# Performance work log

Hardware: AMD Instinct MI355X
Metric: run time of the kernel (lower is better)

## Reference

```python
import jax, jax.numpy as jnp
import numpy as np

H = 1024      # hidden_size
NH = 16       # num_heads
HD = H // NH  # head_dim
E = 4096      # expand_size
EPS = 1e-5


def layernorm(x, w, b):
    mu = jnp.mean(x, axis=-1, keepdims=True)
    var = jnp.mean(jnp.square(x - mu), axis=-1, keepdims=True)
    return (x - mu) * jax.lax.rsqrt(var + EPS) * w + b


def setup_inputs() -> dict:
    key = jax.random.key(0)
    ks = jax.random.split(key, 8)
    s = 1.0 / np.sqrt(H)
    return {
        "x": jax.random.normal(ks[0], (4, 2048, H), dtype=jnp.float32),
        "ln1_w": jnp.ones((H,), jnp.float32),
        "ln1_b": jnp.zeros((H,), jnp.float32),
        "Wqkv": jax.random.normal(ks[1], (H, 3 * H), dtype=jnp.float32) * s,
        "bqkv": jnp.zeros((3 * H,), jnp.float32),
        "Wo": jax.random.normal(ks[2], (H, H), dtype=jnp.float32) * s,
        "bo": jnp.zeros((H,), jnp.float32),
        "ln2_w": jnp.ones((H,), jnp.float32),
        "ln2_b": jnp.zeros((H,), jnp.float32),
        "fc1_w": jax.random.normal(ks[3], (H, E), dtype=jnp.float32) * s,
        "fc1_b": jnp.zeros((E,), jnp.float32),
        "fc2_w": jax.random.normal(ks[4], (E, H), dtype=jnp.float32) * (1.0 / np.sqrt(E)),
        "fc2_b": jnp.zeros((H,), jnp.float32),
    }


def reference(x, ln1_w, ln1_b, Wqkv, bqkv, Wo, bo, ln2_w, ln2_b, fc1_w, fc1_b, fc2_w, fc2_b):
    B, S, C = x.shape
    # --- attention sub-block (pre-norm) ---
    h = layernorm(x, ln1_w, ln1_b)
    qkv = h @ Wqkv + bqkv                             # [B,S,3C]
    qkv = qkv.reshape(B, S, 3, NH, HD)
    q, k, v = (jnp.moveaxis(qkv[:, :, i], 2, 1) for i in range(3))  # [B,NH,S,HD]
    attn = jnp.einsum("bhqd,bhkd->bhqk", q, k) / np.sqrt(HD)        # [B,NH,S,S]
    attn = jax.nn.softmax(attn, axis=-1)
    o = jnp.einsum("bhqk,bhkd->bhqd", attn, v)        # [B,NH,S,HD]
    o = jnp.moveaxis(o, 1, 2).reshape(B, S, C)
    x = x + o @ Wo + bo
    # --- FFN sub-block (pre-norm) ---
    h = layernorm(x, ln2_w, ln2_b)
    h = jax.nn.gelu(h @ fc1_w + fc1_b, approximate=False)
    return x + h @ fc2_w + fc2_b
```

## Files before the change

kernel.cpp:

```cpp
#include <hip/hip_runtime.h>
#include <hip/hip_bf16.h>
#include <math.h>

typedef __bf16 bf16_t;
typedef __bf16 bf16x4 __attribute__((ext_vector_type(4)));
typedef short  s16x8  __attribute__((ext_vector_type(8)));
typedef float  f32x4  __attribute__((ext_vector_type(4)));
typedef float  f32x16 __attribute__((ext_vector_type(16)));

#define DEVINL __device__ __forceinline__

DEVINL void gload_lds16(const void* g, void* l) {
  __builtin_amdgcn_global_load_lds(
      (const __attribute__((address_space(1))) unsigned int*)g,
      (__attribute__((address_space(3))) unsigned int*)l, 16, 0, 0);
}

DEVINL f32x4 mfma16(s16x8 a, s16x8 b, f32x4 c) {
  return __builtin_amdgcn_mfma_f32_16x16x32_bf16(a, b, c, 0, 0, 0);
}

DEVINL f32x16 mfma32(s16x8 a, s16x8 b, f32x16 c) {
  return __builtin_amdgcn_mfma_f32_32x32x16_bf16(a, b, c, 0, 0, 0);
}

DEVINL float fexp2(float x) { return __builtin_amdgcn_exp2f(x); }

__global__ __launch_bounds__(256) void tcast_kernel(const float* __restrict__ W,
                                                    bf16_t* __restrict__ WT,
                                                    int K, int N) {
  __shared__ float tile[32][33];
  const int n0 = blockIdx.x * 32, k0 = blockIdx.y * 32;
  const int tx = threadIdx.x, ty = threadIdx.y;
#pragma unroll
  for (int j = 0; j < 4; ++j)
    tile[ty + j * 8][tx] = W[(size_t)(k0 + ty + j * 8) * N + (n0 + tx)];
  __syncthreads();
#pragma unroll
  for (int j = 0; j < 4; ++j)
    WT[(size_t)(n0 + ty + j * 8) * K + (k0 + tx)] = (bf16_t)tile[tx][ty + j * 8];
}

__global__ __launch_bounds__(256) void ln_kernel(const float* __restrict__ x,
                                                 const float* __restrict__ w,
                                                 const float* __restrict__ b,
                                                 bf16_t* __restrict__ out) {
  const int row = blockIdx.x, tid = threadIdx.x;
  const float4 v = ((const float4*)(x + (size_t)row * 1024))[tid];
  float s  = v.x + v.y + v.z + v.w;
  float s2 = v.x * v.x + v.y * v.y + v.z * v.z + v.w * v.w;
#pragma unroll
  for (int off = 32; off > 0; off >>= 1) {
    s  += __shfl_down(s, off);
    s2 += __shfl_down(s2, off);
  }
  __shared__ float red[8];
  const int wave = tid >> 6, lane = tid & 63;
  if (lane == 0) { red[wave] = s; red[4 + wave] = s2; }
  __syncthreads();
  s  = red[0] + red[1] + red[2] + red[3];
  s2 = red[4] + red[5] + red[6] + red[7];
  const float mu = s * (1.0f / 1024.0f);
  const float rs = rsqrtf(s2 * (1.0f / 1024.0f) - mu * mu + 1e-5f);
  const float4 wv = ((const float4*)w)[tid];
  const float4 bv = ((const float4*)b)[tid];
  bf16x4 o;
  o[0] = (bf16_t)((v.x - mu) * rs * wv.x + bv.x);
  o[1] = (bf16_t)((v.y - mu) * rs * wv.y + bv.y);
  o[2] = (bf16_t)((v.z - mu) * rs * wv.z + bv.z);
  o[3] = (bf16_t)((v.w - mu) * rs * wv.w + bv.w);
  ((bf16x4*)(out + (size_t)row * 1024))[tid] = o;
}

template <int EPI>
__global__ __launch_bounds__(256, 4) void gemm128b(const bf16_t* __restrict__ A,
                                                   const bf16_t* __restrict__ BT,
                                                   const float* __restrict__ bias,
                                                   const float* __restrict__ resid,
                                                   void* __restrict__ out,
                                                   void* __restrict__ out2,
                                                   int M, int N, int K) {
  __shared__ __align__(16) bf16_t sA[128 * 64];
  __shared__ __align__(16) bf16_t sB[128 * 64];
  const int tid = threadIdx.x;
  const int lane = tid & 63, wave = tid >> 6;
  const int wr = wave >> 1, wc = wave & 1;
  const int g = lane >> 4, lr = lane & 15;

  const int bid = blockIdx.x;
  const int cpx = gridDim.x >> 3;
  const int gid = (bid & 7) * cpx + (bid >> 3);
  const int m0 = (gid & 63) * 128, n0 = (gid >> 6) * 128;
  const bf16_t* Ab = A + (size_t)m0 * K;
  const bf16_t* Bb = BT + (size_t)n0 * K;

  f32x4 acc[4][4] = {};

  for (int kt = 0; kt < K; kt += 64) {
    __syncthreads();
#pragma unroll
    for (int q = 0; q < 4; ++q) {
      const int c = q * 256 + tid;
      const int r = c >> 3;
      const int j = (c & 7) ^ (r & 7);
      const size_t doff = (size_t)(q * 256 + wave * 64) * 8;
      gload_lds16(Ab + (size_t)r * K + kt + j * 8, sA + doff);
      gload_lds16(Bb + (size_t)r * K + kt + j * 8, sB + doff);
    }
    __syncthreads();
#pragma unroll
    for (int ks = 0; ks < 2; ++ks) {
      s16x8 af[4], bfr[4];
#pragma unroll
      for (int m = 0; m < 4; ++m) {
        const int r = wr * 64 + m * 16 + lr;
        af[m] = *(const s16x8*)&sA[r * 64 + (((ks << 2) + g) ^ (r & 7)) * 8];
      }
#pragma unroll
      for (int n = 0; n < 4; ++n) {
        const int r = wc * 64 + n * 16 + lr;
        bfr[n] = *(const s16x8*)&sB[r * 64 + (((ks << 2) + g) ^ (r & 7)) * 8];
      }
#pragma unroll
      for (int m = 0; m < 4; ++m)
#pragma unroll
        for (int n = 0; n < 4; ++n)
          acc[m][n] = mfma16(af[m], bfr[n], acc[m][n]);
    }
  }

#pragma unroll
  for (int m = 0; m < 4; ++m)
#pragma unroll
    for (int n = 0; n < 4; ++n) {
      const int col = n0 + wc * 64 + n * 16 + lr;
      const float bv = bias[col];
      const int rrow0 = m0 + wr * 64 + m * 16 + g * 4;
      if (EPI == 3 && col >= 2048) {
        const int col2 = col - 2048;
        bf16x4 pk;
#pragma unroll
        for (int i = 0; i < 4; ++i) pk[i] = (bf16_t)(acc[m][n][i] + bv);
        const size_t didx =
            ((((size_t)(rrow0 >> 11)) * 16 + (col2 >> 6)) * 64 + (col2 & 63)) * 2048 +
            (rrow0 & 2047);
        *(bf16x4*)&((bf16_t*)out2)[didx] = pk;
      } else {
#pragma unroll
        for (int i = 0; i < 4; ++i) {
          const int rrow = rrow0 + i;
          float v = acc[m][n][i] + bv;
          if (EPI == 1) {
            const size_t idx = (size_t)rrow * N + col;
            v += resid[idx];
            ((float*)out)[idx] = v;
          } else if (EPI == 2) {
            v = 0.5f * v * (1.0f + erff(v * 0.70710678118f));
            ((bf16_t*)out)[(size_t)rrow * N + col] = (bf16_t)v;
          } else if (EPI == 3) {
            ((bf16_t*)out)[(size_t)rrow * 2048 + col] = (bf16_t)v;
          } else {
            ((bf16_t*)out)[(size_t)rrow * N + col] = (bf16_t)v;
          }
        }
      }
    }
}

__global__ __launch_bounds__(256) void flash_attn8(const bf16_t* __restrict__ qk,
                                                   const bf16_t* __restrict__ vt,
                                                   bf16_t* __restrict__ O) {
  const int S = 2048;
  const int bid = blockIdx.x;
  const int swz = (bid & 7) * 128 + (bid >> 3);
  const int bh = swz >> 4;
  const int qt = swz & 15;
  const int h = bh & 15;
  const size_t rowbase = (size_t)(bh >> 4) * S;
  const int tid = threadIdx.x, lane = tid & 63, wave = tid >> 6;
  const int ql = lane & 31;
  const int H = lane >> 5;
  const int q0w = qt * 128 + wave * 32;
  const float c2 = 0.18033688f;

  __shared__ __align__(16) bf16_t sK[64 * 64];
  __shared__ __align__(16) bf16_t sVT[64 * 64];
  __shared__ __align__(16) bf16_t sP[4][32 * 64];

  const bf16_t* vtb = vt + (size_t)bh * 64 * 2048;

  s16x8 qf[4];
  {
    const bf16_t* qrow = qk + (rowbase + q0w + ql) * 2048 + h * 64 + 8 * H;
#pragma unroll
    for (int ks = 0; ks < 4; ++ks) qf[ks] = *(const s16x8*)(qrow + 16 * ks);
  }

  f32x16 oa[2] = {};
  float m2 = -1e30f, lrun = 0.0f;

  for (int kv0 = 0; kv0 < S; kv0 += 64) {
    __syncthreads();
#pragma unroll
    for (int p = 0; p < 2; ++p) {
      const int c = p * 256 + wave * 64 + lane;
      const int r = c >> 3;
      const int pb = (c & 7) ^ (r & 7);
      char* dK = (char*)sK + (size_t)(p * 256 + wave * 64) * 16;
      char* dV = (char*)sVT + (size_t)(p * 256 + wave * 64) * 16;
      gload_lds16(qk + (rowbase + kv0 + r) * 2048 + 1024 + h * 64 + pb * 8, dK);
      gload_lds16(vtb + (size_t)r * 2048 + kv0 + pb * 8, dV);
    }
    __syncthreads();

    f32x16 sc[2] = {};
#pragma unroll
    for (int ks = 0; ks < 4; ++ks)
#pragma unroll
      for (int kvf = 0; kvf < 2; ++kvf) {
        const int R = kvf * 32 + ql;
        const s16x8 ak = *(const s16x8*)&sK[R * 64 + (((2 * ks + H) ^ (R & 7)) * 8)];
        sc[kvf] = mfma32(ak, qf[ks], sc[kvf]);
      }

    float rmax = sc[0][0];
#pragma unroll
    for (int f = 0; f < 2; ++f)
#pragma unroll
      for (int r = 0; r < 16; ++r) rmax = fmaxf(rmax, sc[f][r]);
    rmax = fmaxf(rmax, __shfl_xor(rmax, 32));
    const float pm2 = rmax * c2;
    if (!__all(pm2 <= m2 + 8.0f)) {
      const float mn = fmaxf(m2, pm2);
      const float alpha = fexp2(m2 - mn);
      m2 = mn;
      lrun *= alpha;
#pragma unroll
      for (int f = 0; f < 2; ++f)
#pragma unroll
        for (int r = 0; r < 16; ++r) oa[f][r] *= alpha;
    }
    float rsum = 0.0f;
#pragma unroll
    for (int f = 0; f < 2; ++f)
#pragma unroll
      for (int r = 0; r < 16; ++r) {
        const float pp = fexp2(fmaf(sc[f][r], c2, -m2));
        sc[f][r] = pp;
        rsum += pp;
      }
    rsum += __shfl_xor(rsum, 32);
    lrun += rsum;

#pragma unroll
    for (int ks = 0; ks < 4; ++ks)
#pragma unroll
      for (int hi = 0; hi < 2; ++hi) {
        const int f = ks >> 1, rb = 8 * (ks & 1) + 4 * hi;
        bf16x4 pk;
#pragma unroll
        for (int e = 0; e < 4; ++e) pk[e] = (bf16_t)sc[f][rb + e];
        const int slot = ((2 * ks + hi) + ql) & 7;
        *(bf16x4*)&sP[wave][ql * 64 + slot * 8 + 4 * H] = pk;
      }

#pragma unroll
    for (int ks = 0; ks < 4; ++ks) {
      const s16x8 pbf = *(const s16x8*)&sP[wave][ql * 64 + (((2 * ks + H) + ql) & 7) * 8];
#pragma unroll
      for (int df = 0; df < 2; ++df) {
        const int R = df * 32 + ql;
        const s16x8 va = *(const s16x8*)&sVT[R * 64 + (((2 * ks + H) ^ (R & 7)) * 8)];
        oa[df] = mfma32(va, pbf, oa[df]);
      }
    }
  }

  const float rl = 1.0f / lrun;
#pragma unroll
  for (int df = 0; df < 2; ++df)
#pragma unroll
    for (int rr = 0; rr < 4; ++rr) {
      bf16x4 ov;
#pragma unroll
      for (int e = 0; e < 4; ++e) ov[e] = (bf16_t)(oa[df][4 * rr + e] * rl);
      const int d0 = 32 * df + 8 * rr + 4 * H;
      *(bf16x4*)&O[(rowbase + q0w + ql) * 1024 + h * 64 + d0] = ov;
    }
}

extern "C" void kernel_launch(void* const* d_in, const int* in_sizes, int n_in,
                              void* d_out, int out_size, void* d_ws, size_t ws_size,
                              hipStream_t stream) {
  const float* x    = (const float*)d_in[0];
  const float* ln1w = (const float*)d_in[1];
  const float* ln1b = (const float*)d_in[2];
  const float* Wqkv = (const float*)d_in[3];
  const float* bqkv = (const float*)d_in[4];
  const float* Wo   = (const float*)d_in[5];
  const float* bo   = (const float*)d_in[6];
  const float* ln2w = (const float*)d_in[7];
  const float* ln2b = (const float*)d_in[8];
  const float* fc1w = (const float*)d_in[9];
  const float* fc1b = (const float*)d_in[10];
  const float* fc2w = (const float*)d_in[11];
  const float* fc2b = (const float*)d_in[12];

  const int M = 8192;

  char* ws = (char*)d_ws;
  size_t off = 0;
  auto alloc = [&](size_t bytes) {
    char* p = ws + off;
    off += (bytes + 255) & ~(size_t)255;
    return p;
  };
  bf16_t* WqkvT = (bf16_t*)alloc((size_t)3072 * 1024 * 2);
  bf16_t* WoT   = (bf16_t*)alloc((size_t)1024 * 1024 * 2);
  bf16_t* fc1T  = (bf16_t*)alloc((size_t)4096 * 1024 * 2);
  bf16_t* fc2T  = (bf16_t*)alloc((size_t)1024 * 4096 * 2);
  bf16_t* h1    = (bf16_t*)alloc((size_t)M * 1024 * 2);
  bf16_t* qkQK  = (bf16_t*)alloc((size_t)M * 2048 * 2);
  bf16_t* vTg   = (bf16_t*)alloc((size_t)M * 1024 * 2);
  bf16_t* attnO = (bf16_t*)alloc((size_t)M * 1024 * 2);
  float*  x2    = (float*)alloc((size_t)M * 1024 * 4);
  bf16_t* h2   = h1;
  bf16_t* gbuf = qkQK;
  if (off > ws_size) return;

  const dim3 tb(32, 8);
  tcast_kernel<<<dim3(96, 32), tb, 0, stream>>>(Wqkv, WqkvT, 1024, 3072);
  tcast_kernel<<<dim3(32, 32), tb, 0, stream>>>(Wo, WoT, 1024, 1024);
  tcast_kernel<<<dim3(128, 32), tb, 0, stream>>>(fc1w, fc1T, 1024, 4096);
  tcast_kernel<<<dim3(32, 128), tb, 0, stream>>>(fc2w, fc2T, 4096, 1024);

  ln_kernel<<<M, 256, 0, stream>>>(x, ln1w, ln1b, h1);

  gemm128b<3><<<dim3(1536), 256, 0, stream>>>(h1, WqkvT, bqkv, nullptr, qkQK, vTg, M, 3072, 1024);

  flash_attn8<<<dim3(1024), 256, 0, stream>>>(qkQK, vTg, attnO);

  gemm128b<1><<<dim3(512), 256, 0, stream>>>(attnO, WoT, bo, x, x2, nullptr, M, 1024, 1024);

  ln_kernel<<<M, 256, 0, stream>>>(x2, ln2w, ln2b, h2);

  gemm128b<2><<<dim3(2048), 256, 0, stream>>>(h2, fc1T, fc1b, nullptr, gbuf, nullptr, M, 4096, 1024);

  gemm128b<1><<<dim3(512), 256, 0, stream>>>(gbuf, fc2T, fc2b, x2, (float*)d_out, nullptr, M, 1024, 4096);
}
```

Before: 433.3 us.

## Double-buffer LDS tiles in GEMM to overlap global loads with MFMA compute

Converts the bf16 GEMM kernel to use two LDS buffers for the A and B tiles. It issues the async global-to-LDS load for the next K tile before computing on the current one, and drops to one barrier per iteration. The aim is to hide global memory latency behind MFMA work. In exchange LDS per block doubles to 64KB and launch bounds drop from 4 to 2 blocks per SM, which lowers occupancy.

```diff
diff --git a/kernel.cpp b/kernel.cpp
--- a/kernel.cpp
+++ b/kernel.cpp
@@ -73,15 +73,15 @@
 }
 
 template <int EPI>
-__global__ __launch_bounds__(256, 4) void gemm128b(const bf16_t* __restrict__ A,
+__global__ __launch_bounds__(256, 2) void gemm128p(const bf16_t* __restrict__ A,
                                                    const bf16_t* __restrict__ BT,
                                                    const float* __restrict__ bias,
                                                    const float* __restrict__ resid,
                                                    void* __restrict__ out,
                                                    void* __restrict__ out2,
                                                    int M, int N, int K) {
-  __shared__ __align__(16) bf16_t sA[128 * 64];
-  __shared__ __align__(16) bf16_t sB[128 * 64];
+  __shared__ __align__(16) bf16_t sA[2][128 * 64];
+  __shared__ __align__(16) bf16_t sB[2][128 * 64];
   const int tid = threadIdx.x;
   const int lane = tid & 63, wave = tid >> 6;
   const int wr = wave >> 1, wc = wave & 1;
@@ -95,31 +95,38 @@
   const bf16_t* Bb = BT + (size_t)n0 * K;
 
   f32x4 acc[4][4] = {};
-
-  for (int kt = 0; kt < K; kt += 64) {
-    __syncthreads();
+  const int T = K >> 6;
+
+  auto stage = [&](int kt, int buf) {
 #pragma unroll
     for (int q = 0; q < 4; ++q) {
       const int c = q * 256 + tid;
       const int r = c >> 3;
       const int j = (c & 7) ^ (r & 7);
       const size_t doff = (size_t)(q * 256 + wave * 64) * 8;
-      gload_lds16(Ab + (size_t)r * K + kt + j * 8, sA + doff);
-      gload_lds16(Bb + (size_t)r * K + kt + j * 8, sB + doff);
-    }
-    __syncthreads();
+      gload_lds16(Ab + (size_t)r * K + kt + j * 8, &sA[buf][doff]);
+      gload_lds16(Bb + (size_t)r * K + kt + j * 8, &sB[buf][doff]);
+    }
+  };
+
+  stage(0, 0);
+  __syncthreads();
+
+  for (int t = 0; t < T; ++t) {
+    const int cur = t & 1;
+    if (t + 1 < T) stage((t + 1) << 6, cur ^ 1);
 #pragma unroll
     for (int ks = 0; ks < 2; ++ks) {
       s16x8 af[4], bfr[4];
 #pragma unroll
       for (int m = 0; m < 4; ++m) {
         const int r = wr * 64 + m * 16 + lr;
-        af[m] = *(const s16x8*)&sA[r * 64 + (((ks << 2) + g) ^ (r & 7)) * 8];
+        af[m] = *(const s16x8*)&sA[cur][r * 64 + (((ks << 2) + g) ^ (r & 7)) * 8];
       }
 #pragma unroll
       for (int n = 0; n < 4; ++n) {
         const int r = wc * 64 + n * 16 + lr;
-        bfr[n] = *(const s16x8*)&sB[r * 64 + (((ks << 2) + g) ^ (r & 7)) * 8];
+        bfr[n] = *(const s16x8*)&sB[cur][r * 64 + (((ks << 2) + g) ^ (r & 7)) * 8];
       }
 #pragma unroll
       for (int m = 0; m < 4; ++m)
@@ -127,6 +134,7 @@
         for (int n = 0; n < 4; ++n)
           acc[m][n] = mfma16(af[m], bfr[n], acc[m][n]);
     }
+    __syncthreads();
   }
 
 #pragma unroll
@@ -336,15 +344,15 @@
 
   ln_kernel<<<M, 256, 0, stream>>>(x, ln1w, ln1b, h1);
 
-  gemm128b<3><<<dim3(1536), 256, 0, stream>>>(h1, WqkvT, bqkv, nullptr, qkQK, vTg, M, 3072, 1024);
+  gemm128p<3><<<dim3(1536), 256, 0, stream>>>(h1, WqkvT, bqkv, nullptr, qkQK, vTg, M, 3072, 1024);
 
   flash_attn8<<<dim3(1024), 256, 0, stream>>>(qkQK, vTg, attnO);
 
-  gemm128b<1><<<dim3(512), 256, 0, stream>>>(attnO, WoT, bo, x, x2, nullptr, M, 1024, 1024);
+  gemm128p<1><<<dim3(512), 256, 0, stream>>>(attnO, WoT, bo, x, x2, nullptr, M, 1024, 1024);
 
   ln_kernel<<<M, 256, 0, stream>>>(x2, ln2w, ln2b, h2);
 
-  gemm128b<2><<<dim3(2048), 256, 0, stream>>>(h2, fc1T, fc1b, nullptr, gbuf, nullptr, M, 4096, 1024);
-
-  gemm128b<1><<<dim3(512), 256, 0, stream>>>(gbuf, fc2T, fc2b, x2, (float*)d_out, nullptr, M, 1024, 4096);
-}
+  gemm128p<2><<<dim3(2048), 256, 0, stream>>>(h2, fc1T, fc1b, nullptr, gbuf, nullptr, M, 4096, 1024);
+
+  gemm128p<1><<<dim3(512), 256, 0, stream>>>(gbuf, fc2T, fc2b, x2, (float*)d_out, nullptr, M, 1024, 4096);
+}
```

After: 452.4 us. +4.4%, slower.
